# Performance work log

Hardware: AMD Instinct MI355X
Metric: run time of the kernel (lower is better)

## Reference

```python
import jax, jax.numpy as jnp
import numpy as np

T, H, I, E = 1024, 2048, 1408, 32
TOPK, N_GROUP, TOPK_GROUP = 6, 4, 2
ROUTED_SCALE = 2.5  # config.routed_scaling_factor


def setup_inputs() -> dict:
    key = jax.random.key(0)
    ks = jax.random.split(key, 9)
    s = 0.02
    return {
        "hidden_states": jax.random.normal(ks[0], (T, H), jnp.float32),
        "gate_w": jax.random.normal(ks[1], (E, H), jnp.float32) * s,   # router linear weight
        "e_bias": jax.random.normal(ks[2], (E,), jnp.float32) * s,     # e_score_correction_bias
        "w_gate": jax.random.normal(ks[3], (E, H, I), jnp.float32) * s,
        "w_up": jax.random.normal(ks[4], (E, H, I), jnp.float32) * s,
        "w_down": jax.random.normal(ks[5], (E, I, H), jnp.float32) * s,
        "sw_gate": jax.random.normal(ks[6], (H, I), jnp.float32) * s,  # shared expert
        "sw_up": jax.random.normal(ks[7], (H, I), jnp.float32) * s,
        "sw_down": jax.random.normal(ks[8], (I, H), jnp.float32) * s,
    }


def _grouped_topk(scores, e_bias):
    """DeepSeek-V3 'noaux_tc' grouped top-k: sigmoid scores, bias-corrected
    selection, group pruning via sum of per-group top-2, renormalized weights
    taken from the UNbiased scores."""
    sfc = scores + e_bias[None, :]                         # [T,E] scores_for_choice
    g = sfc.reshape(T, N_GROUP, E // N_GROUP)
    top2, _ = jax.lax.top_k(g, 2)
    group_scores = top2.sum(-1)                            # [T, n_group]
    _, gidx = jax.lax.top_k(group_scores, TOPK_GROUP)      # [T, topk_group]
    gmask = jax.nn.one_hot(gidx, N_GROUP, dtype=scores.dtype).sum(1)  # [T, n_group]
    emask = jnp.repeat(gmask, E // N_GROUP, axis=1)        # [T, E]
    masked = jnp.where(emask > 0, sfc, -jnp.inf)
    _, topk_ids = jax.lax.top_k(masked, TOPK)              # [T, topk]
    topk_w = jnp.take_along_axis(scores, topk_ids, axis=1) # gather unbiased scores
    topk_w = topk_w / (topk_w.sum(-1, keepdims=True) + 1e-20)  # renormalize=True
    return topk_w, topk_ids


def reference(hidden_states, gate_w, e_bias, w_gate, w_up, w_down, sw_gate, sw_up, sw_down):
    x = hidden_states  # [T,H]
    # shared expert SwiGLU MLP (gate_up_proj -> npu_swiglu -> down_proj)
    shared = (jax.nn.silu(x @ sw_gate) * (x @ sw_up)) @ sw_down  # [T,H]
    # router
    logits = x @ gate_w.T                                        # [T,E]
    scores = jax.nn.sigmoid(logits.astype(jnp.float32))
    topk_w, topk_ids = _grouped_topk(scores, e_bias)
    # FusedMoE: dispatch/grouped-GEMM/combine, expressed densely via a
    # scatter of top-k weights into a [T,E] combine matrix (zeros for
    # unselected experts), matching the fused kernel's math exactly.
    combine = jnp.zeros((T, E), x.dtype).at[jnp.arange(T)[:, None], topk_ids].add(
        topk_w.astype(x.dtype))
    g = jnp.einsum('th,ehi->tei', x, w_gate)   # [T,E,I]
    u = jnp.einsum('th,ehi->tei', x, w_up)
    h = jax.nn.silu(g) * u
    expert_out = jnp.einsum('tei,eih->teh', h, w_down)  # [T,E,H]
    routed = jnp.einsum('te,teh->th', combine, expert_out)
    return routed * ROUTED_SCALE + shared
```

## Files before the change

kernel.cpp:

```cpp
#include <hip/hip_runtime.h>
#include <cstdint>

#define T 1024
#define H 2048
#define II 1408
#define E 32
#define TOPK 6
#define NGRP 4
#define GSZ 8
#define CAP 1024
#define CAPH 384

typedef __attribute__((ext_vector_type(8))) short short8;
typedef __attribute__((ext_vector_type(4))) float f32x4;
typedef __attribute__((ext_vector_type(2))) unsigned int u32x2;
typedef __attribute__((ext_vector_type(4))) unsigned short us4;

static __device__ __forceinline__ unsigned short f2bf(float f) {
    unsigned int u = __builtin_bit_cast(unsigned int, f);
    u += 0x7FFFu + ((u >> 16) & 1u);
    return (unsigned short)(u >> 16);
}

static __device__ __forceinline__ unsigned int cvtpk(float lo, float hi) {
    unsigned int r;
    asm("v_cvt_pk_bf16_f32 %0, %1, %2" : "=v"(r) : "v"(lo), "v"(hi));
    return r;
}

__global__ void prep_kernel(const float* __restrict__ x, unsigned short* __restrict__ xbf,
                            int* __restrict__ list, float* __restrict__ wts,
                            int* __restrict__ cnt) {
    int gid = blockIdx.x * blockDim.x + threadIdx.x;
    const int n4 = T * H / 4;
    if (gid < n4) {
        const float4 v = reinterpret_cast<const float4*>(x)[gid];
        us4 o;
        o.x = f2bf(v.x); o.y = f2bf(v.y); o.z = f2bf(v.z); o.w = f2bf(v.w);
        reinterpret_cast<us4*>(xbf)[gid] = o;
    }
    if (gid < T) { list[E * CAP + gid] = gid; wts[E * CAP + gid] = 1.0f; }
    if (gid < E + 1) cnt[gid] = (gid == E) ? T : 0;
}

__global__ __launch_bounds__(256) void router_kernel(
        const float* __restrict__ x, const float* __restrict__ gw,
        const float* __restrict__ bias, int* __restrict__ list,
        float* __restrict__ wts, int* __restrict__ cnt) {
    int t = blockIdx.x;
    int tid = threadIdx.x;
    int e = tid >> 3, p = tid & 7;
    const float4* xr = reinterpret_cast<const float4*>(x + (size_t)t * H);
    const float4* gr = reinterpret_cast<const float4*>(gw + (size_t)e * H);
    float part = 0.f;
    for (int q = 0; q < 64; ++q) {
        int idx = p * 64 + q;
        float4 a = xr[idx], b = gr[idx];
        part += a.x * b.x + a.y * b.y + a.z * b.z + a.w * b.w;
    }
    __shared__ float red[256];
    __shared__ float sc[E], sfc[E];
    red[tid] = part;
    __syncthreads();
    if (tid < E) {
        float s = 0.f;
        for (int j = 0; j < 8; ++j) s += red[tid * 8 + j];
        float sig = 1.f / (1.f + expf(-s));
        sc[tid] = sig;
        sfc[tid] = sig + bias[tid];
    }
    __syncthreads();
    if (tid == 0) {
        float gs[NGRP];
        for (int g = 0; g < NGRP; ++g) {
            float m1 = -INFINITY, m2 = -INFINITY;
            for (int j = 0; j < GSZ; ++j) {
                float v = sfc[g * GSZ + j];
                if (v > m1) { m2 = m1; m1 = v; }
                else if (v > m2) m2 = v;
            }
            gs[g] = m1 + m2;
        }
        int g1 = 0;
        for (int g = 1; g < NGRP; ++g) if (gs[g] > gs[g1]) g1 = g;
        int g2 = -1;
        for (int g = 0; g < NGRP; ++g) {
            if (g == g1) continue;
            if (g2 < 0 || gs[g] > gs[g2]) g2 = g;
        }
        int sel[TOPK];
        unsigned int usedmask = 0;
        float wsum = 0.f;
        for (int k = 0; k < TOPK; ++k) {
            float best = -INFINITY; int bi = -1;
            for (int ee = 0; ee < E; ++ee) {
                int g = ee >> 3;
                if (g != g1 && g != g2) continue;
                if (usedmask & (1u << ee)) continue;
                if (sfc[ee] > best) { best = sfc[ee]; bi = ee; }
            }
            usedmask |= (1u << bi);
            sel[k] = bi;
            wsum += sc[bi];
        }
        float fac = 2.5f / (wsum + 1e-20f);
        for (int k = 0; k < TOPK; ++k) {
            int ee = sel[k];
            int pos = atomicAdd(&cnt[ee], 1);
            list[ee * CAP + pos] = t;
            wts[ee * CAP + pos] = sc[ee] * fac;
        }
    }
}

__global__ __launch_bounds__(256, 3) void passA_kernel(
        const unsigned short* __restrict__ xbf,
        const float* __restrict__ wgate, const float* __restrict__ wup,
        const float* __restrict__ swgate, const float* __restrict__ swup,
        const int* __restrict__ list, const int* __restrict__ cnt,
        unsigned short* __restrict__ h) {
    int bx = blockIdx.x;
    int ve, start, end;
    if (bx < E) { ve = bx; start = 0; end = cnt[ve]; }
    else        { ve = E; start = (bx - E) * 256; end = start + 256; }
    if (start >= end) return;
    const int i0 = blockIdx.y * 32;
    const int tid = threadIdx.x, wave = tid >> 6, lane = tid & 63;
    const int lcol = lane & 15, lkg = lane >> 4;
    const int mat = tid >> 7;
    const int wcq = tid & 7;
    const int wkq = (tid >> 3) & 15;
    const float* G = (ve < E) ? wgate + (size_t)ve * H * II : swgate;
    const float* U = (ve < E) ? wup   + (size_t)ve * H * II : swup;
    const float* Wsrc = (mat ? U : G) + (size_t)(wkq * 4) * II + i0 + wcq * 4;
    __shared__ unsigned short lB[2][2][32 * 64];
    __shared__ int tokL[256];
    const int slotbase = (ve < E) ? ve * CAPH : E * CAPH;

#define STAGE_A(BUF) { \
        char* dst = (char*)&lB[BUF][mat][0]; \
        _Pragma("unroll") \
        for (int c = 0; c < 4; ++c) { \
            int ii = wcq * 4 + c; \
            unsigned int ad = ((unsigned)ii * 128 + (unsigned)wkq * 8) ^ (((unsigned)(ii & 7)) << 4); \
            u32x2 pk; \
            pk[0] = cvtpk(pf[0][c], pf[1][c]); \
            pk[1] = cvtpk(pf[2][c], pf[3][c]); \
            *reinterpret_cast<u32x2*>(dst + ad) = pk; \
        } }

    for (int m0 = start; m0 < end; m0 += 256) {
        int msize = min(256, end - m0);
        tokL[tid] = (tid < msize) ? list[ve * CAP + m0 + tid] : 0;
        f32x4 accg[4][2] = {};
        f32x4 accu[4][2] = {};
        f32x4 pf[4];
        #pragma unroll
        for (int q = 0; q < 4; ++q)
            pf[q] = *reinterpret_cast<const f32x4*>(Wsrc + (size_t)q * II);
        STAGE_A(0)
        __syncthreads();
        const unsigned short* xrow[4];
        #pragma unroll
        for (int m = 0; m < 4; ++m)
            xrow[m] = xbf + (size_t)tokL[wave * 64 + m * 16 + lcol] * H;
        bool wact = (wave * 64) < msize;

        for (int ks = 0; ks < 32; ++ks) {
            const int cur = ks & 1;
            const int k0 = ks * 64;
            short8 a[2][4];
            if (wact) {
                #pragma unroll
                for (int s = 0; s < 2; ++s)
                    #pragma unroll
                    for (int m = 0; m < 4; ++m)
                        a[s][m] = *reinterpret_cast<const short8*>(&xrow[m][k0 + s * 32 + lkg * 8]);
            }
            __builtin_amdgcn_sched_barrier(0);
            if (ks + 1 < 32) {
                const float* src = Wsrc + (size_t)((ks + 1) * 64) * II;
                #pragma unroll
                for (int q = 0; q < 4; ++q)
                    pf[q] = *reinterpret_cast<const f32x4*>(src + (size_t)q * II);
            }
            __builtin_amdgcn_sched_barrier(0);
            if (wact) {
                const char* b0 = (const char*)&lB[cur][0][0];
                const char* b1 = (const char*)&lB[cur][1][0];
                #pragma unroll
                for (int s = 0; s < 2; ++s) {
                    #pragma unroll
                    for (int n = 0; n < 2; ++n) {
                        unsigned int ra = ((unsigned)(n * 16 + lcol) * 128 + (unsigned)(s * 64 + lkg * 16))
                                        ^ (((unsigned)(lcol & 7)) << 4);
                        const short8 bg = *reinterpret_cast<const short8*>(b0 + ra);
                        const short8 bu = *reinterpret_cast<const short8*>(b1 + ra);
                        #pragma unroll
                        for (int m = 0; m < 4; ++m) {
                            accg[m][n] = __builtin_amdgcn_mfma_f32_16x16x32_bf16(a[s][m], bg, accg[m][n], 0, 0, 0);
                            accu[m][n] = __builtin_amdgcn_mfma_f32_16x16x32_bf16(a[s][m], bu, accu[m][n], 0, 0, 0);
                        }
                    }
                }
            }
            if (ks + 1 < 32) STAGE_A(cur ^ 1)
            __syncthreads();
        }
        if (wact) {
            #pragma unroll
            for (int m = 0; m < 4; ++m)
                #pragma unroll
                for (int n = 0; n < 2; ++n)
                    #pragma unroll
                    for (int r = 0; r < 4; ++r) {
                        int rowl = wave * 64 + m * 16 + lkg * 4 + r;
                        int pos = m0 + rowl;
                        bool ok = (rowl < msize) && !(ve < E && pos >= CAPH);
                        float gv = accg[m][n][r], uv = accu[m][n][r];
                        float hv = gv / (1.f + expf(-gv)) * uv;
                        if (ok)
                            h[(size_t)(slotbase + pos) * II + i0 + n * 16 + lcol] = f2bf(hv);
                    }
        }
        __syncthreads();
    }
#undef STAGE_A
}

__global__ __launch_bounds__(256, 3) void passB_kernel(
        const unsigned short* __restrict__ h,
        const float* __restrict__ wdown, const float* __restrict__ swdown,
        const int* __restrict__ list, const float* __restrict__ wts,
        const int* __restrict__ cnt, float* __restrict__ out) {
    int bx = blockIdx.x;
    int ve, start, end;
    if (bx < E) { ve = bx; start = 0; end = cnt[ve]; }
    else        { ve = E; start = (bx - E) * 256; end = start + 256; }
    if (start >= end) return;
    const float* W = (ve < E) ? wdown + (size_t)ve * II * H : swdown;
    const int n0 = blockIdx.y * 64;
    const int tid = threadIdx.x, wave = tid >> 6, lane = tid & 63;
    const int lcol = lane & 15, lkg = lane >> 4;
    const int wnq = tid & 15;
    const int wkq = tid >> 4;
    const float* Wsrc = W + (size_t)(wkq * 4) * H + n0 + wnq * 4;
    __shared__ unsigned short lW[2][64 * 64];
    __shared__ int tokL[256];
    __shared__ float wtL[256];
    const int slotbase = (ve < E) ? ve * CAPH : E * CAPH;
    const int NS = II / 64;

#define STAGE_B(BUF) { \
        char* dst = (char*)&lW[BUF][0]; \
        _Pragma("unroll") \
        for (int c = 0; c < 4; ++c) { \
            int nn = wnq * 4 + c; \
            unsigned int ad = ((unsigned)nn * 128 + (unsigned)wkq * 8) ^ (((unsigned)(nn & 7)) << 4); \
            u32x2 pk; \
            pk[0] = cvtpk(pf[0][c], pf[1][c]); \
            pk[1] = cvtpk(pf[2][c], pf[3][c]); \
            *reinterpret_cast<u32x2*>(dst + ad) = pk; \
        } }

    for (int m0 = start; m0 < end; m0 += 256) {
        int msize = min(256, end - m0);
        tokL[tid] = (tid < msize) ? list[ve * CAP + m0 + tid] : 0;
        wtL[tid]  = (tid < msize) ? wts[ve * CAP + m0 + tid] : 0.f;
        f32x4 acc[4][4] = {};
        f32x4 pf[4];
        #pragma unroll
        for (int q = 0; q < 4; ++q)
            pf[q] = *reinterpret_cast<const f32x4*>(Wsrc + (size_t)q * H);
        STAGE_B(0)
        __syncthreads();
        const unsigned short* hrow[4];
        #pragma unroll
        for (int m = 0; m < 4; ++m)
            hrow[m] = h + (size_t)(slotbase + m0 + wave * 64 + m * 16 + lcol) * II;
        bool wact = (wave * 64) < msize;

        for (int ks = 0; ks < NS; ++ks) {
            const int cur = ks & 1;
            const int k0 = ks * 64;
            short8 a[2][4];
            if (wact) {
                #pragma unroll
                for (int s = 0; s < 2; ++s)
                    #pragma unroll
                    for (int m = 0; m < 4; ++m)
                        a[s][m] = *reinterpret_cast<const short8*>(&hrow[m][k0 + s * 32 + lkg * 8]);
            }
            __builtin_amdgcn_sched_barrier(0);
            if (ks + 1 < NS) {
                const float* src = Wsrc + (size_t)((ks + 1) * 64) * H;
                #pragma unroll
                for (int q = 0; q < 4; ++q)
                    pf[q] = *reinterpret_cast<const f32x4*>(src + (size_t)q * H);
            }
            __builtin_amdgcn_sched_barrier(0);
            if (wact) {
                const char* bw0 = (const char*)&lW[cur][0];
                #pragma unroll
                for (int s = 0; s < 2; ++s) {
                    #pragma unroll
                    for (int n = 0; n < 4; ++n) {
                        unsigned int ra = ((unsigned)(n * 16 + lcol) * 128 + (unsigned)(s * 64 + lkg * 16))
                                        ^ (((unsigned)(lcol & 7)) << 4);
                        const short8 b = *reinterpret_cast<const short8*>(bw0 + ra);
                        #pragma unroll
                        for (int m = 0; m < 4; ++m)
                            acc[m][n] = __builtin_amdgcn_mfma_f32_16x16x32_bf16(a[s][m], b, acc[m][n], 0, 0, 0);
                    }
                }
            }
            if (ks + 1 < NS) STAGE_B(cur ^ 1)
            __syncthreads();
        }
        if (wact) {
            #pragma unroll
            for (int m = 0; m < 4; ++m)
                #pragma unroll
                for (int n = 0; n < 4; ++n)
                    #pragma unroll
                    for (int r = 0; r < 4; ++r) {
                        int rowl = wave * 64 + m * 16 + lkg * 4 + r;
                        if (rowl < msize) {
                            int tok = tokL[rowl];
                            float wv = wtL[rowl];
                            unsafeAtomicAdd(&out[(size_t)tok * H + n0 + n * 16 + lcol],
                                            acc[m][n][r] * wv);
                        }
                    }
        }
        __syncthreads();
    }
#undef STAGE_B
}

extern "C" void kernel_launch(void* const* d_in, const int* in_sizes, int n_in,
                              void* d_out, int out_size, void* d_ws, size_t ws_size,
                              hipStream_t stream) {
    const float* x       = (const float*)d_in[0];
    const float* gate_w  = (const float*)d_in[1];
    const float* e_bias  = (const float*)d_in[2];
    const float* w_gate  = (const float*)d_in[3];
    const float* w_up    = (const float*)d_in[4];
    const float* w_down  = (const float*)d_in[5];
    const float* sw_gate = (const float*)d_in[6];
    const float* sw_up   = (const float*)d_in[7];
    const float* sw_down = (const float*)d_in[8];
    float* out = (float*)d_out;

    char* ws = (char*)d_ws;
    unsigned short* xbf = (unsigned short*)ws;
    int*   list = (int*)(ws + 4194304);
    float* wts  = (float*)(ws + 4194304 + 135168);
    int*   cnt  = (int*)(ws + 4194304 + 2 * 135168);
    unsigned short* h = (unsigned short*)(ws + 4194304 + 2 * 135168 + 256);

    hipMemsetAsync(d_out, 0, (size_t)T * H * sizeof(float), stream);
    prep_kernel<<<dim3(2048), dim3(256), 0, stream>>>(x, xbf, list, wts, cnt);
    router_kernel<<<dim3(T), dim3(256), 0, stream>>>(x, gate_w, e_bias, list, wts, cnt);
    passA_kernel<<<dim3(36, 44), dim3(256), 0, stream>>>(xbf, w_gate, w_up, sw_gate, sw_up, list, cnt, h);
    passB_kernel<<<dim3(36, 32), dim3(256), 0, stream>>>(h, w_down, sw_down, list, wts, cnt, out);
}
```

Baseline: 513.0 us.

## Use 512-thread workgroups with XCD-aware block remap in expert GEMM passes

Both grouped-GEMM passes switch from 256 to 512-thread workgroups, so each wave handles 32 rows instead of 64. Each thread stages fewer weight rows per K-step, which cuts per-thread prefetch registers and raises occupancy. A 1-D grid is remapped so that consecutive logical tiles of the same expert land on the same XCD (index modulo 8) for better L2 reuse of the weights. The MFMA section is wrapped in s_setprio and __syncthreads is replaced by an explicit lgkmcnt wait plus s_barrier. The trade-off is more waves competing for the same LDS tile, and smaller per-wave M tiles that lower MFMA-to-load reuse.

```diff
diff --git a/kernel.cpp b/kernel.cpp
--- a/kernel.cpp
+++ b/kernel.cpp
@@ -13,7 +13,6 @@
 
 typedef __attribute__((ext_vector_type(8))) short short8;
 typedef __attribute__((ext_vector_type(4))) float f32x4;
-typedef __attribute__((ext_vector_type(2))) unsigned int u32x2;
 typedef __attribute__((ext_vector_type(4))) unsigned short us4;
 
 static __device__ __forceinline__ unsigned short f2bf(float f) {
@@ -27,6 +26,11 @@
     asm("v_cvt_pk_bf16_f32 %0, %1, %2" : "=v"(r) : "v"(lo), "v"(hi));
     return r;
 }
+
+#define KBAR() { \
+        asm volatile("s_waitcnt lgkmcnt(0)" ::: "memory"); \
+        __builtin_amdgcn_s_barrier(); \
+        __builtin_amdgcn_sched_barrier(0); }
 
 __global__ void prep_kernel(const float* __restrict__ x, unsigned short* __restrict__ xbf,
                             int* __restrict__ list, float* __restrict__ wts,
@@ -113,81 +117,81 @@
     }
 }
 
-__global__ __launch_bounds__(256, 3) void passA_kernel(
+__global__ __launch_bounds__(512, 4) void passA_kernel(
         const unsigned short* __restrict__ xbf,
         const float* __restrict__ wgate, const float* __restrict__ wup,
         const float* __restrict__ swgate, const float* __restrict__ swup,
         const int* __restrict__ list, const int* __restrict__ cnt,
         unsigned short* __restrict__ h) {
-    int bx = blockIdx.x;
+    int wg = blockIdx.x;
+    int logical = (wg & 7) * 198 + (wg >> 3);
+    int bx = logical / 44;
+    int iy = logical - bx * 44;
     int ve, start, end;
     if (bx < E) { ve = bx; start = 0; end = cnt[ve]; }
     else        { ve = E; start = (bx - E) * 256; end = start + 256; }
     if (start >= end) return;
-    const int i0 = blockIdx.y * 32;
+    const int i0 = iy * 32;
     const int tid = threadIdx.x, wave = tid >> 6, lane = tid & 63;
     const int lcol = lane & 15, lkg = lane >> 4;
-    const int mat = tid >> 7;
-    const int wcq = tid & 7;
-    const int wkq = (tid >> 3) & 15;
+    const int mat = tid >> 8;
+    const int sub = tid & 255;
+    const int wiq = sub & 7;
+    const int wkq = sub >> 3;
     const float* G = (ve < E) ? wgate + (size_t)ve * H * II : swgate;
     const float* U = (ve < E) ? wup   + (size_t)ve * H * II : swup;
-    const float* Wsrc = (mat ? U : G) + (size_t)(wkq * 4) * II + i0 + wcq * 4;
+    const float* Wsrc = (mat ? U : G) + (size_t)(wkq * 2) * II + i0 + wiq * 4;
     __shared__ unsigned short lB[2][2][32 * 64];
     __shared__ int tokL[256];
     const int slotbase = (ve < E) ? ve * CAPH : E * CAPH;
 
-#define STAGE_A(BUF) { \
-        char* dst = (char*)&lB[BUF][mat][0]; \
-        _Pragma("unroll") \
-        for (int c = 0; c < 4; ++c) { \
-            int ii = wcq * 4 + c; \
-            unsigned int ad = ((unsigned)ii * 128 + (unsigned)wkq * 8) ^ (((unsigned)(ii & 7)) << 4); \
-            u32x2 pk; \
-            pk[0] = cvtpk(pf[0][c], pf[1][c]); \
-            pk[1] = cvtpk(pf[2][c], pf[3][c]); \
-            *reinterpret_cast<u32x2*>(dst + ad) = pk; \
-        } }
-
     for (int m0 = start; m0 < end; m0 += 256) {
         int msize = min(256, end - m0);
-        tokL[tid] = (tid < msize) ? list[ve * CAP + m0 + tid] : 0;
-        f32x4 accg[4][2] = {};
-        f32x4 accu[4][2] = {};
-        f32x4 pf[4];
+        if (tid < 256) tokL[tid] = (tid < msize) ? list[ve * CAP + m0 + tid] : 0;
+        f32x4 accg[2][2] = {};
+        f32x4 accu[2][2] = {};
+        f32x4 pf0, pf1;
+        {
+            const float* src = Wsrc;
+            pf0 = *reinterpret_cast<const f32x4*>(src);
+            pf1 = *reinterpret_cast<const f32x4*>(src + II);
+            char* dg = (char*)&lB[0][mat][0];
+            #pragma unroll
+            for (int c = 0; c < 4; ++c) {
+                int ii = wiq * 4 + c;
+                unsigned int ad = ((unsigned)ii * 128 + (unsigned)wkq * 4) ^ (((unsigned)(ii & 7)) << 4);
+                *reinterpret_cast<unsigned int*>(dg + ad) = cvtpk(pf0[c], pf1[c]);
+            }
+        }
+        KBAR()
+        const unsigned short* xrow[2];
         #pragma unroll
-        for (int q = 0; q < 4; ++q)
-            pf[q] = *reinterpret_cast<const f32x4*>(Wsrc + (size_t)q * II);
-        STAGE_A(0)
-        __syncthreads();
-        const unsigned short* xrow[4];
-        #pragma unroll
-        for (int m = 0; m < 4; ++m)
-            xrow[m] = xbf + (size_t)tokL[wave * 64 + m * 16 + lcol] * H;
-        bool wact = (wave * 64) < msize;
-
+        for (int m = 0; m < 2; ++m)
+            xrow[m] = xbf + (size_t)tokL[wave * 32 + m * 16 + lcol] * H;
+        bool wact = (wave * 32) < msize;
+
+        #pragma unroll 1
         for (int ks = 0; ks < 32; ++ks) {
             const int cur = ks & 1;
-            const int k0 = ks * 64;
-            short8 a[2][4];
+            short8 a[2][2];
             if (wact) {
                 #pragma unroll
                 for (int s = 0; s < 2; ++s)
                     #pragma unroll
-                    for (int m = 0; m < 4; ++m)
-                        a[s][m] = *reinterpret_cast<const short8*>(&xrow[m][k0 + s * 32 + lkg * 8]);
+                    for (int m = 0; m < 2; ++m)
+                        a[s][m] = *reinterpret_cast<const short8*>(&xrow[m][ks * 64 + s * 32 + lkg * 8]);
             }
             __builtin_amdgcn_sched_barrier(0);
             if (ks + 1 < 32) {
                 const float* src = Wsrc + (size_t)((ks + 1) * 64) * II;
-                #pragma unroll
-                for (int q = 0; q < 4; ++q)
-                    pf[q] = *reinterpret_cast<const f32x4*>(src + (size_t)q * II);
+                pf0 = *reinterpret_cast<const f32x4*>(src);
+                pf1 = *reinterpret_cast<const f32x4*>(src + II);
             }
             __builtin_amdgcn_sched_barrier(0);
             if (wact) {
                 const char* b0 = (const char*)&lB[cur][0][0];
                 const char* b1 = (const char*)&lB[cur][1][0];
+                __builtin_amdgcn_s_setprio(1);
                 #pragma unroll
                 for (int s = 0; s < 2; ++s) {
                     #pragma unroll
@@ -197,24 +201,33 @@
                         const short8 bg = *reinterpret_cast<const short8*>(b0 + ra);
                         const short8 bu = *reinterpret_cast<const short8*>(b1 + ra);
                         #pragma unroll
-                        for (int m = 0; m < 4; ++m) {
+                        for (int m = 0; m < 2; ++m) {
                             accg[m][n] = __builtin_amdgcn_mfma_f32_16x16x32_bf16(a[s][m], bg, accg[m][n], 0, 0, 0);
                             accu[m][n] = __builtin_amdgcn_mfma_f32_16x16x32_bf16(a[s][m], bu, accu[m][n], 0, 0, 0);
                         }
                     }
                 }
-            }
-            if (ks + 1 < 32) STAGE_A(cur ^ 1)
-            __syncthreads();
+                __builtin_amdgcn_s_setprio(0);
+            }
+            if (ks + 1 < 32) {
+                char* dg = (char*)&lB[cur ^ 1][mat][0];
+                #pragma unroll
+                for (int c = 0; c < 4; ++c) {
+                    int ii = wiq * 4 + c;
+                    unsigned int ad = ((unsigned)ii * 128 + (unsigned)wkq * 4) ^ (((unsigned)(ii & 7)) << 4);
+                    *reinterpret_cast<unsigned int*>(dg + ad) = cvtpk(pf0[c], pf1[c]);
+                }
+            }
+            KBAR()
         }
         if (wact) {
             #pragma unroll
-            for (int m = 0; m < 4; ++m)
+            for (int m = 0; m < 2; ++m)
                 #pragma unroll
                 for (int n = 0; n < 2; ++n)
                     #pragma unroll
                     for (int r = 0; r < 4; ++r) {
-                        int rowl = wave * 64 + m * 16 + lkg * 4 + r;
+                        int rowl = wave * 32 + m * 16 + lkg * 4 + r;
                         int pos = m0 + rowl;
                         bool ok = (rowl < msize) && !(ve < E && pos >= CAPH);
                         float gv = accg[m][n][r], uv = accu[m][n][r];
@@ -225,82 +238,82 @@
         }
         __syncthreads();
     }
-#undef STAGE_A
-}
-
-__global__ __launch_bounds__(256, 3) void passB_kernel(
+}
+
+__global__ __launch_bounds__(512, 4) void passB_kernel(
         const unsigned short* __restrict__ h,
         const float* __restrict__ wdown, const float* __restrict__ swdown,
         const int* __restrict__ list, const float* __restrict__ wts,
         const int* __restrict__ cnt, float* __restrict__ out) {
-    int bx = blockIdx.x;
+    int wg = blockIdx.x;
+    int logical = (wg & 7) * 144 + (wg >> 3);
+    int bx = logical / 32;
+    int ny = logical - bx * 32;
     int ve, start, end;
     if (bx < E) { ve = bx; start = 0; end = cnt[ve]; }
     else        { ve = E; start = (bx - E) * 256; end = start + 256; }
     if (start >= end) return;
     const float* W = (ve < E) ? wdown + (size_t)ve * II * H : swdown;
-    const int n0 = blockIdx.y * 64;
+    const int n0 = ny * 64;
     const int tid = threadIdx.x, wave = tid >> 6, lane = tid & 63;
     const int lcol = lane & 15, lkg = lane >> 4;
     const int wnq = tid & 15;
     const int wkq = tid >> 4;
-    const float* Wsrc = W + (size_t)(wkq * 4) * H + n0 + wnq * 4;
+    const float* Wsrc = W + (size_t)(wkq * 2) * H + n0 + wnq * 4;
     __shared__ unsigned short lW[2][64 * 64];
     __shared__ int tokL[256];
     __shared__ float wtL[256];
     const int slotbase = (ve < E) ? ve * CAPH : E * CAPH;
     const int NS = II / 64;
 
-#define STAGE_B(BUF) { \
-        char* dst = (char*)&lW[BUF][0]; \
-        _Pragma("unroll") \
-        for (int c = 0; c < 4; ++c) { \
-            int nn = wnq * 4 + c; \
-            unsigned int ad = ((unsigned)nn * 128 + (unsigned)wkq * 8) ^ (((unsigned)(nn & 7)) << 4); \
-            u32x2 pk; \
-            pk[0] = cvtpk(pf[0][c], pf[1][c]); \
-            pk[1] = cvtpk(pf[2][c], pf[3][c]); \
-            *reinterpret_cast<u32x2*>(dst + ad) = pk; \
-        } }
-
     for (int m0 = start; m0 < end; m0 += 256) {
         int msize = min(256, end - m0);
-        tokL[tid] = (tid < msize) ? list[ve * CAP + m0 + tid] : 0;
-        wtL[tid]  = (tid < msize) ? wts[ve * CAP + m0 + tid] : 0.f;
-        f32x4 acc[4][4] = {};
-        f32x4 pf[4];
+        if (tid < 256) {
+            tokL[tid] = (tid < msize) ? list[ve * CAP + m0 + tid] : 0;
+            wtL[tid]  = (tid < msize) ? wts[ve * CAP + m0 + tid] : 0.f;
+        }
+        f32x4 acc[2][4] = {};
+        f32x4 pf0, pf1;
+        {
+            const float* src = Wsrc;
+            pf0 = *reinterpret_cast<const f32x4*>(src);
+            pf1 = *reinterpret_cast<const f32x4*>(src + H);
+            char* dw = (char*)&lW[0][0];
+            #pragma unroll
+            for (int c = 0; c < 4; ++c) {
+                int nn = wnq * 4 + c;
+                unsigned int ad = ((unsigned)nn * 128 + (unsigned)wkq * 4) ^ (((unsigned)(nn & 7)) << 4);
+                *reinterpret_cast<unsigned int*>(dw + ad) = cvtpk(pf0[c], pf1[c]);
+            }
+        }
+        KBAR()
+        const unsigned short* hrow[2];
         #pragma unroll
-        for (int q = 0; q < 4; ++q)
-            pf[q] = *reinterpret_cast<const f32x4*>(Wsrc + (size_t)q * H);
-        STAGE_B(0)
-        __syncthreads();
-        const unsigned short* hrow[4];
-        #pragma unroll
-        for (int m = 0; m < 4; ++m)
-            hrow[m] = h + (size_t)(slotbase + m0 + wave * 64 + m * 16 + lcol) * II;
-        bool wact = (wave * 64) < msize;
-
+        for (int m = 0; m < 2; ++m)
+            hrow[m] = h + (size_t)(slotbase + m0 + wave * 32 + m * 16 + lcol) * II;
+        bool wact = (wave * 32) < msize;
+
+        #pragma unroll 1
         for (int ks = 0; ks < NS; ++ks) {
             const int cur = ks & 1;
-            const int k0 = ks * 64;
-            short8 a[2][4];
+            short8 a[2][2];
             if (wact) {
                 #pragma unroll
                 for (int s = 0; s < 2; ++s)
                     #pragma unroll
-                    for (int m = 0; m < 4; ++m)
-                        a[s][m] = *reinterpret_cast<const short8*>(&hrow[m][k0 + s * 32 + lkg * 8]);
+                    for (int m = 0; m < 2; ++m)
+                        a[s][m] = *reinterpret_cast<const short8*>(&hrow[m][ks * 64 + s * 32 + lkg * 8]);
             }
             __builtin_amdgcn_sched_barrier(0);
             if (ks + 1 < NS) {
                 const float* src = Wsrc + (size_t)((ks + 1) * 64) * H;
-                #pragma unroll
-                for (int q = 0; q < 4; ++q)
-                    pf[q] = *reinterpret_cast<const f32x4*>(src + (size_t)q * H);
+                pf0 = *reinterpret_cast<const f32x4*>(src);
+                pf1 = *reinterpret_cast<const f32x4*>(src + H);
             }
             __builtin_amdgcn_sched_barrier(0);
             if (wact) {
                 const char* bw0 = (const char*)&lW[cur][0];
+                __builtin_amdgcn_s_setprio(1);
                 #pragma unroll
                 for (int s = 0; s < 2; ++s) {
                     #pragma unroll
@@ -309,22 +322,31 @@
                                         ^ (((unsigned)(lcol & 7)) << 4);
                         const short8 b = *reinterpret_cast<const short8*>(bw0 + ra);
                         #pragma unroll
-                        for (int m = 0; m < 4; ++m)
+                        for (int m = 0; m < 2; ++m)
                             acc[m][n] = __builtin_amdgcn_mfma_f32_16x16x32_bf16(a[s][m], b, acc[m][n], 0, 0, 0);
                     }
                 }
-            }
-            if (ks + 1 < NS) STAGE_B(cur ^ 1)
-            __syncthreads();
+                __builtin_amdgcn_s_setprio(0);
+            }
+            if (ks + 1 < NS) {
+                char* dw = (char*)&lW[cur ^ 1][0];
+                #pragma unroll
+                for (int c = 0; c < 4; ++c) {
+                    int nn = wnq * 4 + c;
+                    unsigned int ad = ((unsigned)nn * 128 + (unsigned)wkq * 4) ^ (((unsigned)(nn & 7)) << 4);
+                    *reinterpret_cast<unsigned int*>(dw + ad) = cvtpk(pf0[c], pf1[c]);
+                }
+            }
+            KBAR()
         }
         if (wact) {
             #pragma unroll
-            for (int m = 0; m < 4; ++m)
+            for (int m = 0; m < 2; ++m)
                 #pragma unroll
                 for (int n = 0; n < 4; ++n)
                     #pragma unroll
                     for (int r = 0; r < 4; ++r) {
-                        int rowl = wave * 64 + m * 16 + lkg * 4 + r;
+                        int rowl = wave * 32 + m * 16 + lkg * 4 + r;
                         if (rowl < msize) {
                             int tok = tokL[rowl];
                             float wv = wtL[rowl];
@@ -335,7 +357,6 @@
         }
         __syncthreads();
     }
-#undef STAGE_B
 }
 
 extern "C" void kernel_launch(void* const* d_in, const int* in_sizes, int n_in,
@@ -362,6 +383,6 @@
     hipMemsetAsync(d_out, 0, (size_t)T * H * sizeof(float), stream);
     prep_kernel<<<dim3(2048), dim3(256), 0, stream>>>(x, xbf, list, wts, cnt);
     router_kernel<<<dim3(T), dim3(256), 0, stream>>>(x, gate_w, e_bias, list, wts, cnt);
-    passA_kernel<<<dim3(36, 44), dim3(256), 0, stream>>>(xbf, w_gate, w_up, sw_gate, sw_up, list, cnt, h);
-    passB_kernel<<<dim3(36, 32), dim3(256), 0, stream>>>(h, w_down, sw_down, list, wts, cnt, out);
-}
+    passA_kernel<<<dim3(1584), dim3(512), 0, stream>>>(xbf, w_gate, w_up, sw_gate, sw_up, list, cnt, h);
+    passB_kernel<<<dim3(1152), dim3(512), 0, stream>>>(h, w_down, sw_down, list, wts, cnt, out);
+}
```

New measurement: 559.0 us. 1.09x slower.
